# Kernel optimization log

Hardware: AMD Instinct MI355X
Metric: run time of the kernel (lower is better)

Reference implementation:

```python
import jax, jax.numpy as jnp
import numpy as np

N_NODES = 200000
N_EDGES = 640000
IN_DIM, H1, H2, OUT_DIM = 128, 64, 32, 20


def _glorot(key, shape):
    fan_in, fan_out = shape[0], shape[1]
    lim = float(np.sqrt(6.0 / (fan_in + fan_out)))
    return jax.random.uniform(key, shape, jnp.float32, -lim, lim)


def setup_inputs() -> dict:
    key = jax.random.key(0)
    ks = jax.random.split(key, 8)
    x = jax.random.normal(ks[0], (N_NODES, IN_DIM), jnp.float32)
    edge_index = jax.random.randint(ks[1], (2, N_EDGES), 0, N_NODES, jnp.int64)
    # SAGEConv params: lin_l (neighbor path, with bias), lin_r (root path, no bias)
    return {
        "x": x,
        "edge_index": edge_index,
        "Wl1": _glorot(ks[2], (IN_DIM, H1)), "bl1": jnp.zeros((H1,), jnp.float32),
        "Wr1": _glorot(ks[3], (IN_DIM, H1)),
        "Wl2": _glorot(ks[4], (H1, H2)), "bl2": jnp.zeros((H2,), jnp.float32),
        "Wr2": _glorot(ks[5], (H1, H2)),
        "Wl3": _glorot(ks[6], (H2, OUT_DIM)), "bl3": jnp.zeros((OUT_DIM,), jnp.float32),
        "Wr3": _glorot(ks[7], (H2, OUT_DIM)),
    }


def _sage_conv(x, src, dst, inv_deg, Wl, bl, Wr):
    # mean-aggregate neighbor features: scatter-add x[src] into dst, divide by in-degree
    msgs = x[src]                                            # [E, D] gather
    agg = jax.ops.segment_sum(msgs, dst, num_segments=N_NODES)  # [N, D]
    agg = agg * inv_deg[:, None]                             # mean
    return agg @ Wl + bl + x @ Wr                            # lin_l(agg) + lin_r(x)


def reference(x, edge_index, Wl1, bl1, Wr1, Wl2, bl2, Wr2, Wl3, bl3, Wr3):
    src, dst = edge_index[0], edge_index[1]
    deg = jax.ops.segment_sum(jnp.ones((src.shape[0],), x.dtype), dst,
                              num_segments=N_NODES)
    inv_deg = jnp.where(deg > 0, 1.0 / jnp.maximum(deg, 1.0), 0.0)

    h = jax.nn.relu(_sage_conv(x, src, dst, inv_deg, Wl1, bl1, Wr1))
    # dropout layers are identity in eval mode
    h = jax.nn.relu(_sage_conv(h, src, dst, inv_deg, Wl2, bl2, Wr2))
    return _sage_conv(h, src, dst, inv_deg, Wl3, bl3, Wr3)
```

## Files before the change

### kernel.cpp

```cpp
#include <hip/hip_runtime.h>
#include <hip/hip_bf16.h>


typedef __attribute__((ext_vector_type(8))) short short8;
typedef __attribute__((ext_vector_type(4))) float f32x4;

__device__ inline unsigned short f2b(float x) {
    return __bfloat16_as_ushort(__float2bfloat16(x));
}
__device__ inline float b2f(unsigned short u) {
    return __uint_as_float(((unsigned)u) << 16);
}


__global__ void zero_ints(int* __restrict__ p, int n) {
    int i = blockIdx.x * blockDim.x + threadIdx.x;
    if (i < n) p[i] = 0;
}

__global__ void hist_kernel(const int* __restrict__ dst, int* __restrict__ deg, int E) {
    int i = blockIdx.x * blockDim.x + threadIdx.x;
    if (i < E) atomicAdd(&deg[dst[i]], 1);
}

__global__ void scan_reduce(const int* __restrict__ deg, int* __restrict__ bsum, int n) {
    __shared__ int s[256];
    int i = blockIdx.x * 256 + threadIdx.x;
    s[threadIdx.x] = (i < n) ? deg[i] : 0;
    __syncthreads();
    for (int off = 128; off > 0; off >>= 1) {
        if (threadIdx.x < off) s[threadIdx.x] += s[threadIdx.x + off];
        __syncthreads();
    }
    if (threadIdx.x == 0) bsum[blockIdx.x] = s[0];
}

__global__ void scan_top(int* __restrict__ bsum, int nb) {
    __shared__ int s[1024];
    int t = threadIdx.x;
    int v = (t < nb) ? bsum[t] : 0;
    s[t] = v;
    __syncthreads();
    for (int off = 1; off < 1024; off <<= 1) {
        int add = (t >= off) ? s[t - off] : 0;
        __syncthreads();
        s[t] += add;
        __syncthreads();
    }
    if (t < nb) bsum[t] = s[t] - v;
}

__global__ void scan_final(const int* __restrict__ deg, const int* __restrict__ bsum,
                           int* __restrict__ rowptr, int* __restrict__ cursor,
                           int n, int E) {
    __shared__ int s[256];
    int t = threadIdx.x;
    int i = blockIdx.x * 256 + t;
    int v = (i < n) ? deg[i] : 0;
    s[t] = v;
    __syncthreads();
    for (int off = 1; off < 256; off <<= 1) {
        int add = (t >= off) ? s[t - off] : 0;
        __syncthreads();
        s[t] += add;
        __syncthreads();
    }
    int excl = s[t] - v + bsum[blockIdx.x];
    if (i < n) {
        rowptr[i] = excl;
        cursor[i] = excl;
    }
    if (i == 0) rowptr[n] = E;
}

__global__ void fill_kernel(const int* __restrict__ src, const int* __restrict__ dst,
                            int* __restrict__ cursor, int* __restrict__ csr, int E) {
    int e = blockIdx.x * blockDim.x + threadIdx.x;
    if (e < E) {
        int pos = atomicAdd(&cursor[dst[e]], 1);
        csr[pos] = src[e];
    }
}


template <int DIN, int DP, int DR, int DT2, int CH, int NU,
          bool RELU, bool IN_BF16, bool OUT_BF16>
__launch_bounds__(256, 4)
__global__ void proj_mfma(const void* __restrict__ xv,
                          const float* __restrict__ Wl,
                          const float* __restrict__ Wr,
                          const float* __restrict__ bl,
                          void* __restrict__ pv,
                          void* __restrict__ rv,
                          int n) {
    constexpr int WAVES = 4;
    constexpr int TILES = DT2 / 16;
    constexpr int TW = TILES / CH;
    constexpr int S = DIN / 32;
    constexpr int NCH = TW * S * 64;

    __shared__ unsigned short sF[NCH * 8];

    const int ch   = (CH > 1) ? ((int)blockIdx.x % CH) : 0;
    const int blk  = (int)blockIdx.x / CH;
    const int nblk = (int)gridDim.x / CH;

    const int tid = threadIdx.x;
    for (int chunk = tid; chunk < NCH; chunk += 256) {
        const int lane_c = chunk & 63;
        const int rest = chunk >> 6;
        const int s = rest % S;
        const int t = rest / S;
        const int c = (ch * TW + t) * 16 + (lane_c & 15);
        const int k0 = s * 32 + (lane_c >> 4) * 8;
        short8 pack;
#pragma unroll
        for (int j = 0; j < 8; ++j) {
            float w = 0.f;
            const int k = k0 + j;
            if (c < DP) w = Wl[k * DP + c];
            else if (c < DP + DR) w = Wr[k * DR + (c - DP)];
            pack[j] = (short)f2b(w);
        }
        *reinterpret_cast<short8*>(&sF[(size_t)chunk * 8]) = pack;
    }
    __syncthreads();

    const int wave = tid >> 6, lane = tid & 63;
    const int ng = wave;
    const int q = lane >> 4, ln = lane & 15;
    const int colbase = ch * (TW * 16);

    const unsigned short* fbase = &sF[(size_t)lane * 8];

    int colg[TW];
    float bias[TW];
#pragma unroll
    for (int t = 0; t < TW; ++t) {
        colg[t] = colbase + t * 16 + ln;
        bias[t] = (colg[t] >= DP && colg[t] < DP + DR) ? bl[colg[t] - DP] : 0.0f;
    }

    float4 rf0[NU][2 * S], rf1[NU][2 * S];
    short8 rb0[NU][S], rb1[NU][S];

    auto load_groups = [&](float4 (&rf)[NU][2 * S], short8 (&rb)[NU][S], int nbase) {
#pragma unroll
        for (int g = 0; g < NU; ++g) {
            const int base = nbase + (ng * NU + g) * 16;
            if (base >= n) continue;
            if constexpr (IN_BF16) {
                const unsigned short* xr =
                    (const unsigned short*)xv + (size_t)(base + ln) * DIN + q * 8;
#pragma unroll
                for (int s = 0; s < S; ++s)
                    rb[g][s] = *reinterpret_cast<const short8*>(xr + s * 32);
            } else {
                const float* xr = (const float*)xv + (size_t)(base + ln) * DIN + q * 8;
#pragma unroll
                for (int s = 0; s < S; ++s) {
                    rf[g][2 * s]     = *reinterpret_cast<const float4*>(xr + s * 32);
                    rf[g][2 * s + 1] = *reinterpret_cast<const float4*>(xr + s * 32 + 4);
                }
            }
        }
    };

    auto compute_groups = [&](float4 (&rf)[NU][2 * S], short8 (&rb)[NU][S], int nbase) {
#pragma unroll
        for (int g = 0; g < NU; ++g) {
            const int base = nbase + (ng * NU + g) * 16;
            if (base >= n) continue;
            short8 af[S];
#pragma unroll
            for (int s = 0; s < S; ++s) {
                if constexpr (IN_BF16) {
                    short8 a = rb[g][s];
                    if (RELU) {
#pragma unroll
                        for (int j = 0; j < 8; ++j)
                            a[j] = ((short)a[j] < 0) ? (short)0 : a[j];
                    }
                    af[s] = a;
                } else {
                    float4 v0 = rf[g][2 * s], v1 = rf[g][2 * s + 1];
                    if (RELU) {
                        v0.x = fmaxf(v0.x, 0.0f); v0.y = fmaxf(v0.y, 0.0f);
                        v0.z = fmaxf(v0.z, 0.0f); v0.w = fmaxf(v0.w, 0.0f);
                        v1.x = fmaxf(v1.x, 0.0f); v1.y = fmaxf(v1.y, 0.0f);
                        v1.z = fmaxf(v1.z, 0.0f); v1.w = fmaxf(v1.w, 0.0f);
                    }
                    short8 a;
                    a[0] = (short)f2b(v0.x); a[1] = (short)f2b(v0.y);
                    a[2] = (short)f2b(v0.z); a[3] = (short)f2b(v0.w);
                    a[4] = (short)f2b(v1.x); a[5] = (short)f2b(v1.y);
                    a[6] = (short)f2b(v1.z); a[7] = (short)f2b(v1.w);
                    af[s] = a;
                }
            }

            f32x4 acc[TW];
#pragma unroll
            for (int t = 0; t < TW; ++t) acc[t] = (f32x4){0.f, 0.f, 0.f, 0.f};
#pragma unroll
            for (int s = 0; s < S; ++s)
#pragma unroll
                for (int t = 0; t < TW; ++t) {
                    short8 bf = *reinterpret_cast<const short8*>(
                        fbase + (size_t)(t * S + s) * 512);
                    acc[t] = __builtin_amdgcn_mfma_f32_16x16x32_bf16(
                        af[s], bf, acc[t], 0, 0, 0);
                }

#pragma unroll
            for (int t = 0; t < TW; ++t) {
                const int c = colg[t];
#pragma unroll
                for (int rr = 0; rr < 4; ++rr) {
                    const int row = base + q * 4 + rr;
                    if (c < DP) {
                        if constexpr (OUT_BF16)
                            ((unsigned short*)pv)[(size_t)row * DP + c] = f2b(acc[t][rr]);
                        else
                            ((float*)pv)[(size_t)row * DP + c] = acc[t][rr];
                    } else if (c < DP + DR) {
                        const float v = acc[t][rr] + bias[t];
                        if constexpr (OUT_BF16)
                            ((unsigned short*)rv)[(size_t)row * DR + (c - DP)] = f2b(v);
                        else
                            ((float*)rv)[(size_t)row * DR + (c - DP)] = v;
                    }
                }
            }
        }
    };

    const int npi = WAVES * NU * 16;
    const int stride = nblk * npi;
    int nb = blk * npi;
    if (nb >= n) return;
    load_groups(rf0, rb0, nb);
    while (true) {
        const int nb1 = nb + stride;
        if (nb1 < n) load_groups(rf1, rb1, nb1);
        compute_groups(rf0, rb0, nb);
        nb = nb1;
        if (nb >= n) break;
        const int nb2 = nb + stride;
        if (nb2 < n) load_groups(rf0, rb0, nb2);
        compute_groups(rf1, rb1, nb);
        nb = nb2;
        if (nb >= n) break;
    }
}


template <int D, int L>
__global__ void agg_bf16(const int* __restrict__ rowptr,
                         const int* __restrict__ csr,
                         const unsigned short* __restrict__ p,
                         unsigned short* __restrict__ out,
                         int n) {
    constexpr int RQ = D / 8;
    long long gid = (long long)blockIdx.x * blockDim.x + threadIdx.x;
    int d = (int)(gid / L);
    int l = (int)(gid % L);
    if (d >= n) return;
    int beg = rowptr[d], end = rowptr[d + 1];
    int deg = end - beg;
    if (deg <= 0) return;

    const short8* pr = reinterpret_cast<const short8*>(p);
    float s[8];
#pragma unroll
    for (int j = 0; j < 8; ++j) s[j] = 0.0f;

    int i = beg;
    for (; i + 4 <= end; i += 4) {
        int e0 = csr[i], e1 = csr[i + 1], e2 = csr[i + 2], e3 = csr[i + 3];
        short8 a = pr[(size_t)e0 * RQ + l];
        short8 b = pr[(size_t)e1 * RQ + l];
        short8 c = pr[(size_t)e2 * RQ + l];
        short8 e = pr[(size_t)e3 * RQ + l];
#pragma unroll
        for (int j = 0; j < 8; ++j)
            s[j] += (b2f((unsigned short)a[j]) + b2f((unsigned short)b[j])) +
                    (b2f((unsigned short)c[j]) + b2f((unsigned short)e[j]));
    }
    for (; i < end; ++i) {
        short8 a = pr[(size_t)csr[i] * RQ + l];
#pragma unroll
        for (int j = 0; j < 8; ++j) s[j] += b2f((unsigned short)a[j]);
    }

    const float inv = 1.0f / (float)deg;
    short8* o = reinterpret_cast<short8*>(out) + (size_t)d * RQ + l;
    short8 cur = *o;
#pragma unroll
    for (int j = 0; j < 8; ++j) {
        float v = b2f((unsigned short)cur[j]) + s[j] * inv;
        cur[j] = (short)f2b(v);
    }
    *o = cur;
}

template <int D, int L>
__global__ void agg_f32(const int* __restrict__ rowptr,
                        const int* __restrict__ csr,
                        const float* __restrict__ p,
                        float* __restrict__ out,
                        int n) {
    constexpr int RQ = D / 4;
    long long gid = (long long)blockIdx.x * blockDim.x + threadIdx.x;
    int d = (int)(gid / L);
    int l = (int)(gid % L);
    if (d >= n || l >= RQ) return;
    int beg = rowptr[d], end = rowptr[d + 1];
    int deg = end - beg;
    if (deg <= 0) return;

    const float4* pr = reinterpret_cast<const float4*>(p);
    float sx = 0.f, sy = 0.f, sz = 0.f, sw = 0.f;
    int i = beg;
    for (; i + 4 <= end; i += 4) {
        int s0 = csr[i], s1 = csr[i + 1], s2 = csr[i + 2], s3 = csr[i + 3];
        float4 a = pr[(size_t)s0 * RQ + l];
        float4 b = pr[(size_t)s1 * RQ + l];
        float4 c = pr[(size_t)s2 * RQ + l];
        float4 e = pr[(size_t)s3 * RQ + l];
        sx += (a.x + b.x) + (c.x + e.x);
        sy += (a.y + b.y) + (c.y + e.y);
        sz += (a.z + b.z) + (c.z + e.z);
        sw += (a.w + b.w) + (c.w + e.w);
    }
    for (; i < end; ++i) {
        float4 a = pr[(size_t)csr[i] * RQ + l];
        sx += a.x; sy += a.y; sz += a.z; sw += a.w;
    }
    const float inv = 1.0f / (float)deg;
    float4* o = reinterpret_cast<float4*>(out) + (size_t)d * RQ + l;
    float4 cur = *o;
    cur.x += sx * inv; cur.y += sy * inv;
    cur.z += sz * inv; cur.w += sw * inv;
    *o = cur;
}


extern "C" void kernel_launch(void* const* d_in, const int* in_sizes, int n_in,
                              void* d_out, int out_size, void* d_ws, size_t ws_size,
                              hipStream_t stream) {
    const float* x   = (const float*)d_in[0];
    const int*   ei  = (const int*)d_in[1];
    const float* Wl1 = (const float*)d_in[2];
    const float* bl1 = (const float*)d_in[3];
    const float* Wr1 = (const float*)d_in[4];
    const float* Wl2 = (const float*)d_in[5];
    const float* bl2 = (const float*)d_in[6];
    const float* Wr2 = (const float*)d_in[7];
    const float* Wl3 = (const float*)d_in[8];
    const float* bl3 = (const float*)d_in[9];
    const float* Wr3 = (const float*)d_in[10];
    float* out = (float*)d_out;

    const int N = in_sizes[0] / 128;
    const int E = in_sizes[1] / 2;
    const int* src  = ei;
    const int* dstp = ei + E;

    unsigned short* A1 = (unsigned short*)d_ws;
    unsigned short* Bb = A1 + (size_t)N * 64;
    unsigned short* A2 = Bb + (size_t)N * 64;
    unsigned short* Cb = A2 + (size_t)N * 32;
    float* A3 = (float*)(Cb + (size_t)N * 32);
    int* rowptr = (int*)(A3 + (size_t)N * 20);
    int* csr    = rowptr + (N + 1);

    int* degi   = (int*)A3;
    int* cursor = degi + N;
    int* bsum   = cursor + N;

    const int NB = (N + 255) / 256;

    zero_ints<<<NB, 256, 0, stream>>>(degi, N);
    hist_kernel<<<(E + 255) / 256, 256, 0, stream>>>(dstp, degi, E);
    scan_reduce<<<NB, 256, 0, stream>>>(degi, bsum, N);
    scan_top<<<1, 1024, 0, stream>>>(bsum, NB);
    scan_final<<<NB, 256, 0, stream>>>(degi, bsum, rowptr, cursor, N, E);
    fill_kernel<<<(E + 255) / 256, 256, 0, stream>>>(src, dstp, cursor, csr, E);

    proj_mfma<128, 64, 64, 128, 2, 1, false, false, true><<<2048, 256, 0, stream>>>(
        x, Wl1, Wr1, bl1, A1, Bb, N);
    agg_bf16<64, 8><<<(int)(((long long)N * 8 + 255) / 256), 256, 0, stream>>>(
        rowptr, csr, A1, Bb, N);

    proj_mfma<64, 32, 32, 64, 1, 2, true, true, true><<<1563, 256, 0, stream>>>(
        Bb, Wl2, Wr2, bl2, A2, Cb, N);
    agg_bf16<32, 4><<<(int)(((long long)N * 4 + 255) / 256), 256, 0, stream>>>(
        rowptr, csr, A2, Cb, N);

    proj_mfma<32, 20, 20, 48, 1, 2, true, true, false><<<1563, 256, 0, stream>>>(
        Cb, Wl3, Wr3, bl3, A3, out, N);
    agg_f32<20, 8><<<(int)(((long long)N * 8 + 255) / 256), 256, 0, stream>>>(
        rowptr, csr, A3, out, N);
}
```

Measured before the change: 344.0 us.

## Add dedicated layer-1 projection kernel with async global-to-LDS double buffering

Replaces the generic first-layer projection with a specialized kernel. It streams 32-row tiles of x directly into LDS via global_load_lds, double-buffered so loads of the next tile overlap MFMA compute on the current one. Weights are converted to bf16 once per block into LDS, and blocks are split across two column halves with a swizzled block index. The aim is to hide global memory latency on the largest input read, at the cost of larger LDS use and a persistent-loop grid of 1536 blocks.

Result: slower. 366.3 us (+6.5%).

```diff
diff --git a/kernel.cpp b/kernel.cpp
--- a/kernel.cpp
+++ b/kernel.cpp
@@ -10,6 +10,12 @@
 }
 __device__ inline float b2f(unsigned short u) {
     return __uint_as_float(((unsigned)u) << 16);
+}
+
+__device__ __forceinline__ void gload_lds16(const void* g, void* l) {
+    __builtin_amdgcn_global_load_lds(
+        (const __attribute__((address_space(1))) void*)g,
+        (__attribute__((address_space(3))) void*)l, 16, 0, 0);
 }
 
 
@@ -79,6 +85,130 @@
     if (e < E) {
         int pos = atomicAdd(&cursor[dst[e]], 1);
         csr[pos] = src[e];
+    }
+}
+
+
+__launch_bounds__(256, 4)
+__global__ void proj1_mfma(const float* __restrict__ x,
+                           const float* __restrict__ Wl,
+                           const float* __restrict__ Wr,
+                           const float* __restrict__ bl,
+                           unsigned short* __restrict__ pv,
+                           unsigned short* __restrict__ rv,
+                           int n) {
+    constexpr int S = 4;
+    constexpr int TWB = 4;
+    constexpr int NCH = TWB * S * 64;
+
+    __shared__ unsigned short sW[NCH * 8];
+    __shared__ float sX[2][32 * 128];
+
+    const int b = (int)blockIdx.x;
+    const int ch = (b >> 3) & 1;
+    const int blk = (b & 7) | ((b >> 4) << 3);
+    const int nblk = (int)gridDim.x >> 1;
+
+    const int tid = threadIdx.x;
+    for (int chunk = tid; chunk < NCH; chunk += 256) {
+        const int lane_c = chunk & 63;
+        const int rest = chunk >> 6;
+        const int s = rest % S;
+        const int t = rest / S;
+        const int c = (ch * TWB + t) * 16 + (lane_c & 15);
+        const int k0 = s * 32 + (lane_c >> 4) * 8;
+        short8 pack;
+#pragma unroll
+        for (int j = 0; j < 8; ++j) {
+            const int k = k0 + j;
+            float w = (c < 64) ? Wl[k * 64 + c] : Wr[k * 64 + (c - 64)];
+            pack[j] = (short)f2b(w);
+        }
+        *reinterpret_cast<short8*>(&sW[(size_t)chunk * 8]) = pack;
+    }
+
+    const int wave = tid >> 6, lane = tid & 63;
+    const int rg = wave & 1, cw = wave >> 1;
+    const int q = lane >> 4, ln = lane & 15;
+
+    int colg[2];
+    float bias[2];
+#pragma unroll
+    for (int t = 0; t < 2; ++t) {
+        colg[t] = ch * 64 + (cw * 2 + t) * 16 + ln;
+        bias[t] = (colg[t] >= 64) ? bl[colg[t] - 64] : 0.0f;
+    }
+
+    auto stage = [&](int d, int nb) {
+#pragma unroll
+        for (int i = 0; i < 4; ++i) {
+            const int cbase = wave * 256 + i * 64;
+            const int ci = cbase + lane;
+            int row = nb + (ci >> 5);
+            if (row >= n) row = n - 1;
+            const float* g = x + (size_t)row * 128 + (ci & 31) * 4;
+            char* l = (char*)&sX[d][0] + (size_t)cbase * 16;
+            gload_lds16(g, l);
+        }
+    };
+
+    auto compute = [&](int d, int nb) {
+        const int rowb = nb + rg * 16;
+        f32x4 acc0 = (f32x4){0.f, 0.f, 0.f, 0.f};
+        f32x4 acc1 = (f32x4){0.f, 0.f, 0.f, 0.f};
+        const int bt = cw * 2;
+#pragma unroll
+        for (int s = 0; s < S; ++s) {
+            const float* xr = &sX[d][(rg * 16 + ln) * 128 + s * 32 + q * 8];
+            float4 v0 = *reinterpret_cast<const float4*>(xr);
+            float4 v1 = *reinterpret_cast<const float4*>(xr + 4);
+            short8 a;
+            a[0] = (short)f2b(v0.x); a[1] = (short)f2b(v0.y);
+            a[2] = (short)f2b(v0.z); a[3] = (short)f2b(v0.w);
+            a[4] = (short)f2b(v1.x); a[5] = (short)f2b(v1.y);
+            a[6] = (short)f2b(v1.z); a[7] = (short)f2b(v1.w);
+            short8 bf0 = *reinterpret_cast<const short8*>(
+                &sW[((size_t)(bt * S + s)) * 512 + (size_t)lane * 8]);
+            short8 bf1 = *reinterpret_cast<const short8*>(
+                &sW[((size_t)((bt + 1) * S + s)) * 512 + (size_t)lane * 8]);
+            acc0 = __builtin_amdgcn_mfma_f32_16x16x32_bf16(a, bf0, acc0, 0, 0, 0);
+            acc1 = __builtin_amdgcn_mfma_f32_16x16x32_bf16(a, bf1, acc1, 0, 0, 0);
+        }
+#pragma unroll
+        for (int t = 0; t < 2; ++t) {
+            const f32x4 acc = t ? acc1 : acc0;
+            const int c = colg[t];
+#pragma unroll
+            for (int rr = 0; rr < 4; ++rr) {
+                const int row = rowb + q * 4 + rr;
+                if (row < n) {
+                    if (c < 64)
+                        pv[(size_t)row * 64 + c] = f2b(acc[rr]);
+                    else
+                        rv[(size_t)row * 64 + (c - 64)] = f2b(acc[rr] + bias[t]);
+                }
+            }
+        }
+    };
+
+    constexpr int npi = 32;
+    const int stride = nblk * npi;
+    int nb = blk * npi;
+    if (nb >= n) return;
+    stage(0, nb);
+    __syncthreads();
+    while (true) {
+        const int nb1 = nb + stride;
+        if (nb1 < n) stage(1, nb1);
+        compute(0, nb);
+        __syncthreads();
+        if (nb1 >= n) break;
+        const int nb2 = nb1 + stride;
+        if (nb2 < n) stage(0, nb2);
+        compute(1, nb1);
+        __syncthreads();
+        nb = nb2;
+        if (nb >= n) break;
     }
 }
 
@@ -388,8 +518,7 @@
     scan_final<<<NB, 256, 0, stream>>>(degi, bsum, rowptr, cursor, N, E);
     fill_kernel<<<(E + 255) / 256, 256, 0, stream>>>(src, dstp, cursor, csr, E);
 
-    proj_mfma<128, 64, 64, 128, 2, 1, false, false, true><<<2048, 256, 0, stream>>>(
-        x, Wl1, Wr1, bl1, A1, Bb, N);
+    proj1_mfma<<<1536, 256, 0, stream>>>(x, Wl1, Wr1, bl1, A1, Bb, N);
     agg_bf16<64, 8><<<(int)(((long long)N * 8 + 255) / 256), 256, 0, stream>>>(
         rowptr, csr, A1, Bb, N);
 
```
